# Kernel tuning notes

Hardware: AMD Instinct MI355X
Metric: run time of the kernel (lower is better)

The kernel has to match this reference:

```python
import jax, jax.numpy as jnp
import numpy as np

DIM = 4096          # power of two -> no padding branch
LAYERS = 12         # log2(DIM)
BATCH = 8192


def setup_inputs() -> dict:
    key = jax.random.key(0)
    kx, ka = jax.random.split(key)
    x = jax.random.normal(kx, (BATCH, DIM), dtype=jnp.float32)
    # original init: uniform(-0.05, 0.05) per layer of DIM//2 angles
    angles = jax.random.uniform(ka, (LAYERS, DIM // 2), dtype=jnp.float32,
                                minval=-0.05, maxval=0.05)
    return {"x": x, "angles": angles}


def reference(x, angles):
    """Butterfly O(d log d) rotation. x:(B,d), angles:(L, d//2).

    Layer l pairs elements (j, j+stride), stride=2**l. The torch code's
    angle index for pair offset i in block starting at `start` is
    start//2 + i, which equals reshaping theta to (num_blocks, stride).
    """
    B, d = x.shape
    out = x
    for l in range(LAYERS):
        stride = 1 << l
        nb = d // (2 * stride)              # blocks per layer
        theta = angles[l].reshape(nb, stride)
        c = jnp.cos(theta)                  # (nb, stride)
        s = jnp.sin(theta)
        o = out.reshape(B, nb, 2, stride)
        xl = o[:, :, 0, :]                  # (B, nb, stride)
        xr = o[:, :, 1, :]
        new_l = c * xl + s * xr
        new_r = -s * xl + c * xr
        out = jnp.stack([new_l, new_r], axis=2).reshape(B, d)
    return out
```

## Files before the change

### kernel.cpp

```cpp
#include <hip/hip_runtime.h>


#define DIM    4096
#define LAYERS 12
#define BATCH  8192
#define NANG   2048
#define BLOCK  512

typedef unsigned int u32;

__device__ __forceinline__ int swzQ(int Q) {
    return Q ^ ((Q >> 3) & 7) ^ ((Q >> 6) & 7);
}
__device__ __forceinline__ int perm(int e) {
    return (swzQ(e >> 2) << 2) | (e & 3);
}
__device__ __forceinline__ constexpr int inner_idx(int m, int jj) {
    return ((m >> (jj + 1)) << jj) + (m & ((1 << jj) - 1));
}

__device__ __forceinline__ void rot(float& xl, float& xr, float c, float s) {
    float nl = fmaf(s, xr, c * xl);
    float nr = fmaf(-s, xl, c * xr);
    xl = nl; xr = nr;
}

__global__ void __launch_bounds__(256) cs_kernel(const float* __restrict__ angles,
                                                 float2* __restrict__ T, int n) {
    int i = blockIdx.x * blockDim.x + threadIdx.x;
    if (i >= n) return;
    float a = angles[i];
    float c = cosf(a), s = sinf(a);
    int l = i >> 11, aa = i & 2047;
    int region, jj, t, ii;
    if (l < 3)      { region = 0; jj = l;     t = aa >> 2;  ii = aa & 3; }
    else if (l < 6) { region = 1; jj = l - 3; int B = aa >> 5, r = aa & 31;
                      ii = r >> 3; t = 8 * B + (r & 7); }
    else if (l < 9) { region = 2; jj = l - 6; int S = aa >> 8, r = aa & 255;
                      ii = r >> 6; t = 64 * S + (r & 63); }
    else            { region = 3; jj = l - 9; ii = aa >> 9; t = aa & 511; }
    int f4 = region * 3072 + (jj * 2 + (ii >> 1)) * 512 + t;
    T[f4 * 2 + (ii & 1)] = make_float2(c, s);
}

#define PHASE_ROTS(A, v0, v1)                                              \
    _Pragma("unroll")                                                      \
    for (int jj = 0; jj < 3; ++jj) {                                       \
        const int st = 1 << jj;                                            \
        _Pragma("unroll")                                                  \
        for (int m = 0; m < 8; ++m) {                                      \
            if (!(m & st)) {                                               \
                const int ii = inner_idx(m, jj);                           \
                const float c = (ii & 1) ? A[jj*2+(ii>>1)].z : A[jj*2+(ii>>1)].x; \
                const float s = (ii & 1) ? A[jj*2+(ii>>1)].w : A[jj*2+(ii>>1)].y; \
                rot(v0[m], v0[m + st], c, s);                              \
                rot(v1[m], v1[m + st], c, s);                              \
            }                                                              \
        }                                                                  \
    }

__global__ void __launch_bounds__(BLOCK, 8)
butterfly_kernel(const float* __restrict__ x, const float4* __restrict__ T4,
                 float* __restrict__ out) {
    __shared__ float lds[2 * DIM];
    const int t = threadIdx.x;
    const int wave = t >> 6, lane = t & 63;
    const long row0 = (long)blockIdx.x * 2;

    #pragma unroll
    for (int r = 0; r < 2; ++r) {
        const float* src = x + (row0 + r) * DIM;
        #pragma unroll
        for (int m = 0; m < 2; ++m) {
            const int qbase = 512 * m + 64 * wave;
            const int g = swzQ(qbase + lane);
            __builtin_amdgcn_global_load_lds(
                (const __attribute__((address_space(1))) u32*)(src + 4 * g),
                (__attribute__((address_space(3))) u32*)(lds + r * DIM + 4 * qbase),
                16, 0, 0);
        }
    }
    __syncthreads();

    float v0[8], v1[8];

    {
        const int q0 = 4 * swzQ(2 * t), q1 = 4 * swzQ(2 * t + 1);
        float4 A[6];
        #pragma unroll
        for (int k = 0; k < 6; ++k) A[k] = T4[k * 512 + t];
        float4 a00 = *(const float4*)(lds + q0);
        float4 a01 = *(const float4*)(lds + q1);
        float4 a10 = *(const float4*)(lds + DIM + q0);
        float4 a11 = *(const float4*)(lds + DIM + q1);
        v0[0]=a00.x; v0[1]=a00.y; v0[2]=a00.z; v0[3]=a00.w;
        v0[4]=a01.x; v0[5]=a01.y; v0[6]=a01.z; v0[7]=a01.w;
        v1[0]=a10.x; v1[1]=a10.y; v1[2]=a10.z; v1[3]=a10.w;
        v1[4]=a11.x; v1[5]=a11.y; v1[6]=a11.z; v1[7]=a11.w;
        PHASE_ROTS(A, v0, v1);
        *(float4*)(lds + q0)       = make_float4(v0[0], v0[1], v0[2], v0[3]);
        *(float4*)(lds + q1)       = make_float4(v0[4], v0[5], v0[6], v0[7]);
        *(float4*)(lds + DIM + q0) = make_float4(v1[0], v1[1], v1[2], v1[3]);
        *(float4*)(lds + DIM + q1) = make_float4(v1[4], v1[5], v1[6], v1[7]);
    }
    __syncthreads();

    {
        const int eb = 64 * (t >> 3) + (t & 7);
        float4 A[6];
        #pragma unroll
        for (int k = 0; k < 6; ++k) A[k] = T4[3072 + k * 512 + t];
        int ps[8];
        #pragma unroll
        for (int m = 0; m < 8; ++m) {
            ps[m] = perm(eb + 8 * m);
            v0[m] = lds[ps[m]];
            v1[m] = lds[DIM + ps[m]];
        }
        PHASE_ROTS(A, v0, v1);
        #pragma unroll
        for (int m = 0; m < 8; ++m) {
            lds[ps[m]]       = v0[m];
            lds[DIM + ps[m]] = v1[m];
        }
    }
    __syncthreads();

    {
        const int eb = 512 * (t >> 6) + (t & 63);
        float4 A[6];
        #pragma unroll
        for (int k = 0; k < 6; ++k) A[k] = T4[6144 + k * 512 + t];
        int ps[8];
        #pragma unroll
        for (int m = 0; m < 8; ++m) {
            ps[m] = perm(eb + 64 * m);
            v0[m] = lds[ps[m]];
            v1[m] = lds[DIM + ps[m]];
        }
        PHASE_ROTS(A, v0, v1);
        #pragma unroll
        for (int m = 0; m < 8; ++m) {
            lds[ps[m]]       = v0[m];
            lds[DIM + ps[m]] = v1[m];
        }
    }
    __syncthreads();

    {
        float4 A[6];
        #pragma unroll
        for (int k = 0; k < 6; ++k) A[k] = T4[9216 + k * 512 + t];
        #pragma unroll
        for (int m = 0; m < 8; ++m) {
            const int p = perm(t + 512 * m);
            v0[m] = lds[p];
            v1[m] = lds[DIM + p];
        }
        PHASE_ROTS(A, v0, v1);
        float* o0 = out + row0 * DIM + t;
        float* o1 = o0 + DIM;
        #pragma unroll
        for (int m = 0; m < 8; ++m) {
            o0[m << 9] = v0[m];
            o1[m << 9] = v1[m];
        }
    }
}

extern "C" void kernel_launch(void* const* d_in, const int* in_sizes, int n_in,
                              void* d_out, int out_size, void* d_ws, size_t ws_size,
                              hipStream_t stream) {
    (void)in_sizes; (void)n_in; (void)out_size; (void)ws_size;
    const float* x      = (const float*)d_in[0];
    const float* angles = (const float*)d_in[1];
    float* out = (float*)d_out;

    const int n = LAYERS * NANG;
    cs_kernel<<<(n + 255) / 256, 256, 0, stream>>>(angles, (float2*)d_ws, n);
    butterfly_kernel<<<BATCH / 2, BLOCK, 0, stream>>>(x, (const float4*)d_ws, out);
}
```

Baseline: 61.22 us.

## Interleave two rows as float2 pairs in LDS and use packed rotations

Each thread now reads its first-phase inputs straight from global memory instead of staging them through an async global-to-LDS copy. The two rows of a block are kept in shared memory interleaved as float2 pairs under a new swizzled slot mapping. Rotations work on 2-wide vectors, which can map to packed FMA instructions, and each element exchange becomes one 8-byte LDS access instead of two 4-byte ones. Barriers are replaced by an explicit lgkmcnt wait, a sched_barrier and s_barrier, and angle-table loads are moved after the LDS reads. The risks are a less coalesced direct global load pattern and a different set of bank conflicts.

```diff
diff --git a/kernel.cpp b/kernel.cpp
--- a/kernel.cpp
+++ b/kernel.cpp
@@ -8,20 +8,27 @@
 #define BLOCK  512
 
 typedef unsigned int u32;
+typedef float v2f __attribute__((ext_vector_type(2)));
+
+#define BAR() do {                                             \
+    asm volatile("s_waitcnt lgkmcnt(0)" ::: "memory");         \
+    __builtin_amdgcn_sched_barrier(0);                         \
+    __builtin_amdgcn_s_barrier();                              \
+} while (0)
 
 __device__ __forceinline__ int swzQ(int Q) {
     return Q ^ ((Q >> 3) & 7) ^ ((Q >> 6) & 7);
 }
-__device__ __forceinline__ int perm(int e) {
-    return (swzQ(e >> 2) << 2) | (e & 3);
+__device__ __forceinline__ int uslot(int e) {
+    return 2 * swzQ(e >> 1) + (e & 1);
 }
 __device__ __forceinline__ constexpr int inner_idx(int m, int jj) {
     return ((m >> (jj + 1)) << jj) + (m & ((1 << jj) - 1));
 }
 
-__device__ __forceinline__ void rot(float& xl, float& xr, float c, float s) {
-    float nl = fmaf(s, xr, c * xl);
-    float nr = fmaf(-s, xl, c * xr);
+__device__ __forceinline__ void rot2(v2f& xl, v2f& xr, float c, float s) {
+    v2f nl = c * xl + s * xr;
+    v2f nr = c * xr - s * xl;
     xl = nl; xr = nr;
 }
 
@@ -43,7 +50,7 @@
     T[f4 * 2 + (ii & 1)] = make_float2(c, s);
 }
 
-#define PHASE_ROTS(A, v0, v1)                                              \
+#define PHASE_ROTS(A, w)                                                   \
     _Pragma("unroll")                                                      \
     for (int jj = 0; jj < 3; ++jj) {                                       \
         const int st = 1 << jj;                                            \
@@ -53,8 +60,7 @@
                 const int ii = inner_idx(m, jj);                           \
                 const float c = (ii & 1) ? A[jj*2+(ii>>1)].z : A[jj*2+(ii>>1)].x; \
                 const float s = (ii & 1) ? A[jj*2+(ii>>1)].w : A[jj*2+(ii>>1)].y; \
-                rot(v0[m], v0[m + st], c, s);                              \
-                rot(v1[m], v1[m + st], c, s);                              \
+                rot2(w[m], w[m + st], c, s);                               \
             }                                                              \
         }                                                                  \
     }
@@ -62,108 +68,80 @@
 __global__ void __launch_bounds__(BLOCK, 8)
 butterfly_kernel(const float* __restrict__ x, const float4* __restrict__ T4,
                  float* __restrict__ out) {
-    __shared__ float lds[2 * DIM];
+    __shared__ v2f buf[DIM];
     const int t = threadIdx.x;
-    const int wave = t >> 6, lane = t & 63;
     const long row0 = (long)blockIdx.x * 2;
 
-    #pragma unroll
-    for (int r = 0; r < 2; ++r) {
-        const float* src = x + (row0 + r) * DIM;
-        #pragma unroll
-        for (int m = 0; m < 2; ++m) {
-            const int qbase = 512 * m + 64 * wave;
-            const int g = swzQ(qbase + lane);
-            __builtin_amdgcn_global_load_lds(
-                (const __attribute__((address_space(1))) u32*)(src + 4 * g),
-                (__attribute__((address_space(3))) u32*)(lds + r * DIM + 4 * qbase),
-                16, 0, 0);
-        }
-    }
-    __syncthreads();
-
-    float v0[8], v1[8];
+    v2f w[8];
 
     {
-        const int q0 = 4 * swzQ(2 * t), q1 = 4 * swzQ(2 * t + 1);
+        const float* p0 = x + row0 * DIM + 8 * t;
+        const float* p1 = p0 + DIM;
+        float4 a = *(const float4*)(p0),     b = *(const float4*)(p0 + 4);
+        float4 c = *(const float4*)(p1),     d = *(const float4*)(p1 + 4);
+        w[0] = v2f{a.x, c.x}; w[1] = v2f{a.y, c.y};
+        w[2] = v2f{a.z, c.z}; w[3] = v2f{a.w, c.w};
+        w[4] = v2f{b.x, d.x}; w[5] = v2f{b.y, d.y};
+        w[6] = v2f{b.z, d.z}; w[7] = v2f{b.w, d.w};
         float4 A[6];
         #pragma unroll
         for (int k = 0; k < 6; ++k) A[k] = T4[k * 512 + t];
-        float4 a00 = *(const float4*)(lds + q0);
-        float4 a01 = *(const float4*)(lds + q1);
-        float4 a10 = *(const float4*)(lds + DIM + q0);
-        float4 a11 = *(const float4*)(lds + DIM + q1);
-        v0[0]=a00.x; v0[1]=a00.y; v0[2]=a00.z; v0[3]=a00.w;
-        v0[4]=a01.x; v0[5]=a01.y; v0[6]=a01.z; v0[7]=a01.w;
-        v1[0]=a10.x; v1[1]=a10.y; v1[2]=a10.z; v1[3]=a10.w;
-        v1[4]=a11.x; v1[5]=a11.y; v1[6]=a11.z; v1[7]=a11.w;
-        PHASE_ROTS(A, v0, v1);
-        *(float4*)(lds + q0)       = make_float4(v0[0], v0[1], v0[2], v0[3]);
-        *(float4*)(lds + q1)       = make_float4(v0[4], v0[5], v0[6], v0[7]);
-        *(float4*)(lds + DIM + q0) = make_float4(v1[0], v1[1], v1[2], v1[3]);
-        *(float4*)(lds + DIM + q1) = make_float4(v1[4], v1[5], v1[6], v1[7]);
+        PHASE_ROTS(A, w)
+        #pragma unroll
+        for (int q = 0; q < 4; ++q) {
+            *(float4*)(&buf[2 * swzQ(4 * t + q)]) =
+                make_float4(w[2*q].x, w[2*q].y, w[2*q+1].x, w[2*q+1].y);
+        }
     }
-    __syncthreads();
+    BAR();
 
     {
         const int eb = 64 * (t >> 3) + (t & 7);
+        int ps[8];
+        #pragma unroll
+        for (int m = 0; m < 8; ++m) {
+            ps[m] = uslot(eb + 8 * m);
+            w[m] = buf[ps[m]];
+        }
         float4 A[6];
         #pragma unroll
         for (int k = 0; k < 6; ++k) A[k] = T4[3072 + k * 512 + t];
+        PHASE_ROTS(A, w)
+        #pragma unroll
+        for (int m = 0; m < 8; ++m) buf[ps[m]] = w[m];
+    }
+    BAR();
+
+    {
+        const int eb = 512 * (t >> 6) + (t & 63);
         int ps[8];
         #pragma unroll
         for (int m = 0; m < 8; ++m) {
-            ps[m] = perm(eb + 8 * m);
-            v0[m] = lds[ps[m]];
-            v1[m] = lds[DIM + ps[m]];
+            ps[m] = uslot(eb + 64 * m);
+            w[m] = buf[ps[m]];
         }
-        PHASE_ROTS(A, v0, v1);
-        #pragma unroll
-        for (int m = 0; m < 8; ++m) {
-            lds[ps[m]]       = v0[m];
-            lds[DIM + ps[m]] = v1[m];
-        }
-    }
-    __syncthreads();
-
-    {
-        const int eb = 512 * (t >> 6) + (t & 63);
         float4 A[6];
         #pragma unroll
         for (int k = 0; k < 6; ++k) A[k] = T4[6144 + k * 512 + t];
-        int ps[8];
+        PHASE_ROTS(A, w)
         #pragma unroll
-        for (int m = 0; m < 8; ++m) {
-            ps[m] = perm(eb + 64 * m);
-            v0[m] = lds[ps[m]];
-            v1[m] = lds[DIM + ps[m]];
-        }
-        PHASE_ROTS(A, v0, v1);
-        #pragma unroll
-        for (int m = 0; m < 8; ++m) {
-            lds[ps[m]]       = v0[m];
-            lds[DIM + ps[m]] = v1[m];
-        }
+        for (int m = 0; m < 8; ++m) buf[ps[m]] = w[m];
     }
-    __syncthreads();
+    BAR();
 
     {
+        #pragma unroll
+        for (int m = 0; m < 8; ++m) w[m] = buf[uslot(t + 512 * m)];
         float4 A[6];
         #pragma unroll
         for (int k = 0; k < 6; ++k) A[k] = T4[9216 + k * 512 + t];
-        #pragma unroll
-        for (int m = 0; m < 8; ++m) {
-            const int p = perm(t + 512 * m);
-            v0[m] = lds[p];
-            v1[m] = lds[DIM + p];
-        }
-        PHASE_ROTS(A, v0, v1);
+        PHASE_ROTS(A, w)
         float* o0 = out + row0 * DIM + t;
         float* o1 = o0 + DIM;
         #pragma unroll
         for (int m = 0; m < 8; ++m) {
-            o0[m << 9] = v0[m];
-            o1[m << 9] = v1[m];
+            o0[m << 9] = w[m].x;
+            o1[m << 9] = w[m].y;
         }
     }
 }
```

After: 60.99 us. Within noise of the previous version (-0.4%).
